# Kernel tuning notes

Measured on AMD Instinct MI355X. Metric: run time of the kernel, lower is better.

## Reference

```python
import jax, jax.numpy as jnp
import numpy as np

WS = 8        # window_size
NH = 16       # num_heads

def setup_inputs() -> dict:
    key = jax.random.key(0)
    ks = jax.random.split(key, 6)
    B, H, W, C = 16, 64, 64, 512
    nW = (H // WS) * (W // WS)
    return {
        "x": jax.random.normal(ks[0], (B, H * W, C), jnp.float32),
        "qkv_w": jax.random.normal(ks[1], (3 * C, C), jnp.float32) * 0.02,
        "qkv_b": jax.random.normal(ks[2], (3 * C,), jnp.float32) * 0.02,
        "proj_w": jax.random.normal(ks[3], (C, C), jnp.float32) * 0.02,
        "proj_b": jax.random.normal(ks[4], (C,), jnp.float32) * 0.02,
        "attn_mask": jax.random.normal(ks[5], (nW, WS * WS, WS * WS), jnp.float32),
        "H": H,
        "W": W,
    }

def reference(x, qkv_w, qkv_b, proj_w, proj_b, attn_mask, H, W):
    B, N, C = x.shape
    ws = WS
    hd = C // NH
    scale = hd ** (-0.5)
    x_img = x.reshape(B, H, W, C)
    pad_h = (ws - H % ws) % ws
    pad_w = (ws - W % ws) % ws
    if pad_h > 0 or pad_w > 0:
        x_img = jnp.pad(x_img, ((0, 0), (0, pad_h), (0, pad_w), (0, 0)))
    Hp, Wp = H + pad_h, W + pad_w
    nW = (Hp // ws) * (Wp // ws)
    # window partition: [B*nW, ws*ws, C]
    x_win = x_img.reshape(B, Hp // ws, ws, Wp // ws, ws, C)
    x_win = x_win.transpose(0, 1, 3, 2, 4, 5).reshape(B * nW, ws * ws, C)
    # fused qkv projection (torch Linear: y = x @ W^T + b)
    qkv = x_win @ qkv_w.T + qkv_b
    qkv = qkv.reshape(B * nW, ws * ws, 3, NH, hd).transpose(2, 0, 3, 1, 4)
    q, k, v = qkv[0], qkv[1], qkv[2]  # each [B*nW, NH, ws*ws, hd]
    attn = jnp.einsum('bhqd,bhkd->bhqk', q, k) * scale
    if attn_mask is not None:
        attn = attn.reshape(B, nW, NH, ws * ws, ws * ws)
        attn = attn + attn_mask[None, :, None, :, :]
        attn = attn.reshape(B * nW, NH, ws * ws, ws * ws)
    attn = jax.nn.softmax(attn, axis=-1)
    out = jnp.einsum('bhqk,bhkd->bhqd', attn, v)
    out = out.transpose(0, 2, 1, 3).reshape(B * nW, ws * ws, C)
    out = out @ proj_w.T + proj_b
    # window reverse
    out = out.reshape(B, Hp // ws, Wp // ws, ws, ws, C)
    out = out.transpose(0, 1, 3, 2, 4, 5).reshape(B, Hp, Wp, C)
    out = out[:, :H, :W, :].reshape(B, H * W, C)
    return out
```

## Files before the change

### kernel.cpp

```cpp
#include <hip/hip_runtime.h>


typedef unsigned short u16;
typedef unsigned int u32;
typedef __attribute__((ext_vector_type(8))) u16 u16x8;
typedef __attribute__((ext_vector_type(8))) short short8;
typedef __attribute__((ext_vector_type(4))) float f32x4;

__device__ __forceinline__ u16 f2bf(float f) {
    u32 u = __float_as_uint(f);
    u += 0x7fffu + ((u >> 16) & 1u);
    return (u16)(u >> 16);
}

__device__ __forceinline__ f32x4 MFMA(u16x8 a, u16x8 b, f32x4 c) {
    return __builtin_amdgcn_mfma_f32_16x16x32_bf16(
        __builtin_bit_cast(short8, a), __builtin_bit_cast(short8, b), c, 0, 0, 0);
}

__device__ __forceinline__ void gload16(const void* g, void* l) {
    __builtin_amdgcn_global_load_lds(
        (const __attribute__((address_space(1))) void*)g,
        (__attribute__((address_space(3))) void*)l, 16, 0, 0);
}

__device__ __forceinline__ int win2img(int r) {
    int b = r >> 12;
    int w = (r >> 6) & 63;
    int t = r & 63;
    int img = (((w >> 3) << 3) + (t >> 3)) * 64 + ((w & 7) << 3) + (t & 7);
    return (b << 12) + img;
}

__device__ __forceinline__ u16x8 cvt8(const float* src) {
    float4 a = *(const float4*)src;
    float4 b = *(const float4*)(src + 4);
    u16x8 t;
    t[0] = f2bf(a.x); t[1] = f2bf(a.y); t[2] = f2bf(a.z); t[3] = f2bf(a.w);
    t[4] = f2bf(b.x); t[5] = f2bf(b.y); t[6] = f2bf(b.z); t[7] = f2bf(b.w);
    return t;
}

__global__ __launch_bounds__(256)
void conv_f2b(const float* __restrict__ in, u16* __restrict__ out, int n8) {
    int u = blockIdx.x * 256 + threadIdx.x;
    if (u >= n8) return;
    *(u16x8*)(out + (size_t)u * 8) = cvt8(in + (size_t)u * 8);
}

__global__ __launch_bounds__(256)
void conv_permute_x(const float* __restrict__ x, u16* __restrict__ xw) {
    int u = blockIdx.x * 256 + threadIdx.x;
    int r = u >> 6;
    int c = (u & 63) << 3;
    int g = win2img(r);
    *(u16x8*)(xw + (size_t)r * 512 + c) = cvt8(x + (size_t)g * 512 + c);
}

template<bool PERM_OUT, bool OUT_F32>
__global__ __launch_bounds__(256, 4)
void gemm_bt(const u16* __restrict__ A, const u16* __restrict__ Wt,
             const float* __restrict__ bias, void* __restrict__ C,
             int NB, int Nfull)
{
    __shared__ char lds[32768];

    const int nwg = gridDim.x;
    const int q   = nwg >> 3;
    const int wg  = (blockIdx.x & 7) * q + (blockIdx.x >> 3);
    const int m0  = (wg / NB) * 128;
    const int n0  = (wg % NB) * 128;

    const int tid  = threadIdx.x;
    const int lane = tid & 63;
    const int wv   = tid >> 6;
    const int wm   = (wv >> 1) << 6;
    const int wn   = (wv & 1) << 6;
    const int lr   = lane & 15;
    const int lg   = lane >> 4;

    const int grow  = tid >> 2;
    const int gcolb = (tid & 3) << 4;
    const u32 tb    = (u32)tid << 4;

    const char* aptr = (const char*)A + (((size_t)(m0 + grow)) << 10) + gcolb;
    const char* bptr = (const char*)Wt + (((size_t)(n0 + grow)) << 10) + gcolb;

    f32x4 acc[4][4] = {};

#define STAGE(buf, kt) do {                                                   \
    const int ko_ = (kt) * 64;                                                \
    char* d_ = lds + (buf) * 16384 + tb;                                      \
    gload16(aptr + ko_,              d_);                                     \
    gload16(aptr + (64 << 10) + ko_, d_ + 4096);                              \
    gload16(bptr + ko_,              d_ + 8192);                              \
    gload16(bptr + (64 << 10) + ko_, d_ + 12288);                             \
} while (0)

#define COMPUTE(buf) do {                                                     \
    const u16* As_ = (const u16*)(lds + (buf) * 16384);                       \
    const u16* Bs_ = (const u16*)(lds + (buf) * 16384 + 8192);                \
    u16x8 af_[4], bf_[4];                                                     \
    _Pragma("unroll")                                                         \
    for (int mi = 0; mi < 4; ++mi)                                            \
        af_[mi] = *(const u16x8*)(As_ + (wm + mi * 16 + lr) * 32 + lg * 8);   \
    _Pragma("unroll")                                                         \
    for (int ni = 0; ni < 4; ++ni)                                            \
        bf_[ni] = *(const u16x8*)(Bs_ + (wn + ni * 16 + lr) * 32 + lg * 8);   \
    _Pragma("unroll")                                                         \
    for (int mi = 0; mi < 4; ++mi)                                            \
        _Pragma("unroll")                                                     \
        for (int ni = 0; ni < 4; ++ni)                                        \
            acc[mi][ni] = MFMA(af_[mi], bf_[ni], acc[mi][ni]);                \
} while (0)

    STAGE(0, 0);
    __syncthreads();

#pragma unroll 1
    for (int kt = 0; kt < 16; kt += 2) {
        STAGE(1, kt + 1);
        COMPUTE(0);
        __syncthreads();
        if (kt + 2 < 16) STAGE(0, kt + 2);
        COMPUTE(1);
        __syncthreads();
    }

#undef STAGE
#undef COMPUTE

#pragma unroll
    for (int mi = 0; mi < 4; ++mi) {
#pragma unroll
        for (int ni = 0; ni < 4; ++ni) {
            const int col = n0 + wn + ni * 16 + lr;
            const float bv = bias[col];
#pragma unroll
            for (int r = 0; r < 4; ++r) {
                int gr = m0 + wm + mi * 16 + lg * 4 + r;
                if (PERM_OUT) gr = win2img(gr);
                const float v = acc[mi][ni][r] + bv;
                if constexpr (OUT_F32)
                    ((float*)C)[(size_t)gr * Nfull + col] = v;
                else
                    ((u16*)C)[(size_t)gr * Nfull + col] = f2bf(v);
            }
        }
    }
}

__global__ __launch_bounds__(256, 2)
void attn_kernel(const u16* __restrict__ qkv, const float* __restrict__ mask,
                 u16* __restrict__ attn_out)
{
    __shared__ u16 sP[4][64][72];

    const int tid  = threadIdx.x;
    const int lane = tid & 63;
    const int wv   = tid >> 6;
    const int lr   = lane & 15;
    const int lg   = lane >> 4;
    const int win  = blockIdx.x;
    const int wib  = win & 63;
    const size_t rb = (size_t)win * 64;
    const float* maskp = mask + (size_t)wib * 64 * 64;
    const float scale = 0.17677669529663687f;

    for (int hi = 0; hi < 4; ++hi) {
        const int h = hi * 4 + wv;
        const size_t hoff = (size_t)h * 32;

        u16x8 qf[4], kf[4];
#pragma unroll
        for (int mt = 0; mt < 4; ++mt) {
            const u16* rowp = qkv + (rb + mt * 16 + lr) * 1536 + hoff + lg * 8;
            qf[mt] = *(const u16x8*)rowp;
            kf[mt] = *(const u16x8*)(rowp + 512);
        }
        f32x4 s[4][4] = {};
#pragma unroll
        for (int mi = 0; mi < 4; ++mi)
#pragma unroll
            for (int ni = 0; ni < 4; ++ni)
                s[mi][ni] = MFMA(qf[mi], kf[ni], s[mi][ni]);

        float rsum[4][4];
#pragma unroll
        for (int mi = 0; mi < 4; ++mi) {
#pragma unroll
            for (int r = 0; r < 4; ++r) {
                const int qrow = mi * 16 + lg * 4 + r;
                float vv[4];
                float mx = -1e30f;
#pragma unroll
                for (int ni = 0; ni < 4; ++ni) {
                    const int kcol = ni * 16 + lr;
                    float v = s[mi][ni][r] * scale + maskp[qrow * 64 + kcol];
                    vv[ni] = v;
                    mx = fmaxf(mx, v);
                }
#pragma unroll
                for (int mk = 1; mk <= 8; mk <<= 1)
                    mx = fmaxf(mx, __shfl_xor(mx, mk, 64));
                float sum = 0.f;
#pragma unroll
                for (int ni = 0; ni < 4; ++ni) {
                    float p = __expf(vv[ni] - mx);
                    sum += p;
                    s[mi][ni][r] = p;
                }
#pragma unroll
                for (int mk = 1; mk <= 8; mk <<= 1)
                    sum += __shfl_xor(sum, mk, 64);
                rsum[mi][r] = sum;
            }
        }

        __syncthreads();
#pragma unroll
        for (int mi = 0; mi < 4; ++mi)
#pragma unroll
            for (int ni = 0; ni < 4; ++ni)
#pragma unroll
                for (int r = 0; r < 4; ++r)
                    sP[wv][mi * 16 + lg * 4 + r][ni * 16 + lr] = f2bf(s[mi][ni][r]);
        __syncthreads();

        u16x8 pf[4][2];
#pragma unroll
        for (int mt = 0; mt < 4; ++mt)
#pragma unroll
            for (int k2 = 0; k2 < 2; ++k2)
                pf[mt][k2] = *(const u16x8*)&sP[wv][mt * 16 + lr][k2 * 32 + lg * 8];

        u16x8 vf[2][2];
#pragma unroll
        for (int k2 = 0; k2 < 2; ++k2)
#pragma unroll
            for (int nt = 0; nt < 2; ++nt) {
                const u16* vp = qkv + (rb + k2 * 32 + lg * 8) * 1536 + 1024 + hoff + nt * 16 + lr;
                u16x8 tmp;
#pragma unroll
                for (int j = 0; j < 8; ++j) tmp[j] = vp[(size_t)j * 1536];
                vf[k2][nt] = tmp;
            }

        f32x4 o[4][2] = {};
#pragma unroll
        for (int mt = 0; mt < 4; ++mt)
#pragma unroll
            for (int k2 = 0; k2 < 2; ++k2)
#pragma unroll
                for (int nt = 0; nt < 2; ++nt)
                    o[mt][nt] = MFMA(pf[mt][k2], vf[k2][nt], o[mt][nt]);

#pragma unroll
        for (int mt = 0; mt < 4; ++mt)
#pragma unroll
            for (int nt = 0; nt < 2; ++nt)
#pragma unroll
                for (int r = 0; r < 4; ++r) {
                    const int row = mt * 16 + lg * 4 + r;
                    const int d = nt * 16 + lr;
                    attn_out[(rb + row) * 512 + hoff + d] =
                        f2bf(o[mt][nt][r] / rsum[mt][r]);
                }
    }
}

extern "C" void kernel_launch(void* const* d_in, const int* in_sizes, int n_in,
                              void* d_out, int out_size, void* d_ws, size_t ws_size,
                              hipStream_t stream)
{
    const float* x      = (const float*)d_in[0];
    const float* qkv_w  = (const float*)d_in[1];
    const float* qkv_b  = (const float*)d_in[2];
    const float* proj_w = (const float*)d_in[3];
    const float* proj_b = (const float*)d_in[4];
    const float* mask   = (const float*)d_in[5];
    float* out = (float*)d_out;

    const size_t WQKV  = 1536ull * 512;
    const size_t WPROJ = 512ull * 512;

    u16* wq = (u16*)d_ws;
    u16* wp = wq + WQKV;
    u16* chunk = wp + WPROJ;

    const size_t xwPB  = 4096ull * 512;
    const size_t qkvPB = 4096ull * 1536;
    const size_t attPB = 4096ull * 512;
    const size_t perBatchBytes = (xwPB + qkvPB + attPB) * 2;

    size_t avail = ws_size - (WQKV + WPROJ) * 2;
    int Bc = (int)(avail / perBatchBytes);
    if (Bc > 16) Bc = 16;
    if (Bc < 1) Bc = 1;

    u16* xw_ws  = chunk;
    u16* qkv_ws = xw_ws + (size_t)Bc * xwPB;
    u16* att_ws = qkv_ws + (size_t)Bc * qkvPB;

    conv_f2b<<<dim3((WQKV / 8 + 255) / 256), 256, 0, stream>>>(qkv_w, wq, (int)(WQKV / 8));
    conv_f2b<<<dim3((WPROJ / 8 + 255) / 256), 256, 0, stream>>>(proj_w, wp, (int)(WPROJ / 8));

    for (int b0 = 0; b0 < 16; b0 += Bc) {
        const int bc = (16 - b0) < Bc ? (16 - b0) : Bc;
        const float* xc = x + (size_t)b0 * 4096 * 512;
        float* outc = out + (size_t)b0 * 4096 * 512;

        conv_permute_x<<<dim3(bc * 1024), 256, 0, stream>>>(xc, xw_ws);
        gemm_bt<false, false><<<dim3(bc * 32 * 12), 256, 0, stream>>>(
            xw_ws, wq, qkv_b, qkv_ws, 12, 1536);
        attn_kernel<<<dim3(bc * 64), 256, 0, stream>>>(qkv_ws, mask, att_ws);
        gemm_bt<true, true><<<dim3(bc * 32 * 4), 256, 0, stream>>>(
            att_ws, wp, proj_b, outc, 4, 512);
    }
}
```

Measured before the change: 332.0 us.

## Fuse x conversion into QKV GEMM, write V transposed, stage mask in LDS

Removes the separate conv_permute_x kernel. The QKV GEMM now loads fp32 x rows directly in window order, converts them to bf16 in registers and writes them to LDS, with a K tile of 32. The V part of the QKV output is written transposed per window, so the attention kernel can load V fragments with a single vector load instead of eight strided scalar loads. The attention kernel also stages the mask transposed in LDS and reads it as float4. The cost is that the fp32 A tile is re-read and re-converted by all 12 column blocks, which adds global traffic and an extra sync per K step.

```diff
diff --git a/kernel.cpp b/kernel.cpp
--- a/kernel.cpp
+++ b/kernel.cpp
@@ -3,6 +3,7 @@
 
 typedef unsigned short u16;
 typedef unsigned int u32;
+typedef __attribute__((ext_vector_type(4))) u16 u16x4;
 typedef __attribute__((ext_vector_type(8))) u16 u16x8;
 typedef __attribute__((ext_vector_type(8))) short short8;
 typedef __attribute__((ext_vector_type(4))) float f32x4;
@@ -48,28 +49,19 @@
     *(u16x8*)(out + (size_t)u * 8) = cvt8(in + (size_t)u * 8);
 }
 
-__global__ __launch_bounds__(256)
-void conv_permute_x(const float* __restrict__ x, u16* __restrict__ xw) {
-    int u = blockIdx.x * 256 + threadIdx.x;
-    int r = u >> 6;
-    int c = (u & 63) << 3;
-    int g = win2img(r);
-    *(u16x8*)(xw + (size_t)r * 512 + c) = cvt8(x + (size_t)g * 512 + c);
-}
-
-template<bool PERM_OUT, bool OUT_F32>
-__global__ __launch_bounds__(256, 4)
-void gemm_bt(const u16* __restrict__ A, const u16* __restrict__ Wt,
-             const float* __restrict__ bias, void* __restrict__ C,
-             int NB, int Nfull)
+__global__ __launch_bounds__(256, 3)
+void gemm_qkv(const float* __restrict__ X, const u16* __restrict__ Wq,
+              const float* __restrict__ bias, u16* __restrict__ QK,
+              u16* __restrict__ VT)
 {
-    __shared__ char lds[32768];
+    __shared__ u16 sA[2][128 * 32];
+    __shared__ u16 sB[2][128 * 32];
 
     const int nwg = gridDim.x;
     const int q   = nwg >> 3;
-    const int wg  = (blockIdx.x & 7) * q + (blockIdx.x >> 3);
-    const int m0  = (wg / NB) * 128;
-    const int n0  = (wg % NB) * 128;
+    const int wg  = ((int)blockIdx.x & 7) * q + ((int)blockIdx.x >> 3);
+    const int m0  = (wg / 12) * 128;
+    const int n0  = (wg % 12) * 128;
 
     const int tid  = threadIdx.x;
     const int lane = tid & 63;
@@ -79,12 +71,133 @@
     const int lr   = lane & 15;
     const int lg   = lane >> 4;
 
-    const int grow  = tid >> 2;
-    const int gcolb = (tid & 3) << 4;
-    const u32 tb    = (u32)tid << 4;
-
-    const char* aptr = (const char*)A + (((size_t)(m0 + grow)) << 10) + gcolb;
-    const char* bptr = (const char*)Wt + (((size_t)(n0 + grow)) << 10) + gcolb;
+    const int ar = tid >> 1;
+    const int kh = (tid & 1) << 4;
+    const float* ax = X + ((size_t)win2img(m0 + ar) << 9) + kh;
+    u16* aw = &sA[0][ar * 32 + kh];
+
+    const char* bptr0 = (const char*)Wq + ((size_t)(n0 + (tid >> 2)) << 10) + ((tid & 3) << 4);
+    const char* bptr1 = bptr0 + (64 << 10);
+
+    f32x4 acc[4][4] = {};
+    float4 a0, a1, a2, a3;
+
+#define LOADA(kt) do {                                                        \
+    const float* p_ = ax + (kt) * 32;                                         \
+    a0 = *(const float4*)p_;  a1 = *(const float4*)(p_ + 4);                  \
+    a2 = *(const float4*)(p_ + 8); a3 = *(const float4*)(p_ + 12);            \
+} while (0)
+
+#define WRITEA(buf) do {                                                      \
+    u16x8 t_;                                                                 \
+    t_[0]=f2bf(a0.x); t_[1]=f2bf(a0.y); t_[2]=f2bf(a0.z); t_[3]=f2bf(a0.w);   \
+    t_[4]=f2bf(a1.x); t_[5]=f2bf(a1.y); t_[6]=f2bf(a1.z); t_[7]=f2bf(a1.w);   \
+    *(u16x8*)(aw + (buf) * 4096) = t_;                                        \
+    t_[0]=f2bf(a2.x); t_[1]=f2bf(a2.y); t_[2]=f2bf(a2.z); t_[3]=f2bf(a2.w);   \
+    t_[4]=f2bf(a3.x); t_[5]=f2bf(a3.y); t_[6]=f2bf(a3.z); t_[7]=f2bf(a3.w);   \
+    *(u16x8*)(aw + (buf) * 4096 + 8) = t_;                                    \
+} while (0)
+
+#define STAGEB(buf, kt) do {                                                  \
+    char* d_ = (char*)sB + (buf) * 8192 + tid * 16;                           \
+    gload16(bptr0 + (kt) * 64, d_);                                           \
+    gload16(bptr1 + (kt) * 64, d_ + 4096);                                    \
+} while (0)
+
+#define COMPUTE(buf) do {                                                     \
+    const u16* As_ = &sA[buf][0];                                             \
+    const u16* Bs_ = &sB[buf][0];                                             \
+    u16x8 af_[4], bf_[4];                                                     \
+    _Pragma("unroll")                                                         \
+    for (int mi = 0; mi < 4; ++mi)                                            \
+        af_[mi] = *(const u16x8*)(As_ + (wm + mi * 16 + lr) * 32 + lg * 8);   \
+    _Pragma("unroll")                                                         \
+    for (int ni = 0; ni < 4; ++ni)                                            \
+        bf_[ni] = *(const u16x8*)(Bs_ + (wn + ni * 16 + lr) * 32 + lg * 8);   \
+    _Pragma("unroll")                                                         \
+    for (int mi = 0; mi < 4; ++mi)                                            \
+        _Pragma("unroll")                                                     \
+        for (int ni = 0; ni < 4; ++ni)                                        \
+            acc[mi][ni] = MFMA(af_[mi], bf_[ni], acc[mi][ni]);                \
+} while (0)
+
+    LOADA(0);
+    STAGEB(0, 0);
+    WRITEA(0);
+    __syncthreads();
+
+#pragma unroll 1
+    for (int t = 0; t < 16; ++t) {
+        const int cur = t & 1, nxt = cur ^ 1;
+        if (t < 15) { LOADA(t + 1); STAGEB(nxt, t + 1); }
+        COMPUTE(cur);
+        __syncthreads();
+        if (t < 15) {
+            WRITEA(nxt);
+            __syncthreads();
+        }
+    }
+
+#undef LOADA
+#undef WRITEA
+#undef STAGEB
+#undef COMPUTE
+
+    if (n0 < 1024) {
+#pragma unroll
+        for (int mi = 0; mi < 4; ++mi)
+#pragma unroll
+            for (int ni = 0; ni < 4; ++ni) {
+                const int col = n0 + wn + ni * 16 + lr;
+                const float bv = bias[col];
+#pragma unroll
+                for (int r = 0; r < 4; ++r) {
+                    const int gr = m0 + wm + mi * 16 + lg * 4 + r;
+                    QK[((size_t)gr << 10) + col] = f2bf(acc[mi][ni][r] + bv);
+                }
+            }
+    } else {
+#pragma unroll
+        for (int mi = 0; mi < 4; ++mi) {
+            const int gr0 = m0 + wm + mi * 16 + lg * 4;
+            const int win = gr0 >> 6, ro = gr0 & 63;
+#pragma unroll
+            for (int ni = 0; ni < 4; ++ni) {
+                const int col = n0 + wn + ni * 16 + lr;
+                const float bv = bias[col];
+                const int d = col - 1024;
+                u16x4 h;
+#pragma unroll
+                for (int r = 0; r < 4; ++r) h[r] = f2bf(acc[mi][ni][r] + bv);
+                *(u16x4*)(VT + (((size_t)win << 9) + d) * 64 + ro) = h;
+            }
+        }
+    }
+}
+
+__global__ __launch_bounds__(256, 4)
+void gemm_proj(const u16* __restrict__ A, const u16* __restrict__ Wt,
+               const float* __restrict__ bias, float* __restrict__ C)
+{
+    __shared__ char lds[32768];
+
+    const int nwg = gridDim.x;
+    const int q   = nwg >> 3;
+    const int wg  = ((int)blockIdx.x & 7) * q + ((int)blockIdx.x >> 3);
+    const int m0  = (wg / 4) * 128;
+    const int n0  = (wg % 4) * 128;
+
+    const int tid  = threadIdx.x;
+    const int lane = tid & 63;
+    const int wv   = tid >> 6;
+    const int wm   = (wv >> 1) << 6;
+    const int wn   = (wv & 1) << 6;
+    const int lr   = lane & 15;
+    const int lg   = lane >> 4;
+
+    const char* aptr = (const char*)A + (((size_t)(m0 + (tid >> 2))) << 10) + ((tid & 3) << 4);
+    const char* bptr = (const char*)Wt + (((size_t)(n0 + (tid >> 2))) << 10) + ((tid & 3) << 4);
+    const u32 tb = (u32)tid << 4;
 
     f32x4 acc[4][4] = {};
 
@@ -131,30 +244,25 @@
 #undef COMPUTE
 
 #pragma unroll
-    for (int mi = 0; mi < 4; ++mi) {
+    for (int mi = 0; mi < 4; ++mi)
 #pragma unroll
         for (int ni = 0; ni < 4; ++ni) {
             const int col = n0 + wn + ni * 16 + lr;
             const float bv = bias[col];
 #pragma unroll
             for (int r = 0; r < 4; ++r) {
-                int gr = m0 + wm + mi * 16 + lg * 4 + r;
-                if (PERM_OUT) gr = win2img(gr);
-                const float v = acc[mi][ni][r] + bv;
-                if constexpr (OUT_F32)
-                    ((float*)C)[(size_t)gr * Nfull + col] = v;
-                else
-                    ((u16*)C)[(size_t)gr * Nfull + col] = f2bf(v);
+                const int gr = win2img(m0 + wm + mi * 16 + lg * 4 + r);
+                C[((size_t)gr << 9) + col] = acc[mi][ni][r] + bv;
             }
         }
-    }
 }
 
 __global__ __launch_bounds__(256, 2)
-void attn_kernel(const u16* __restrict__ qkv, const float* __restrict__ mask,
-                 u16* __restrict__ attn_out)
+void attn_kernel(const u16* __restrict__ QK, const u16* __restrict__ VT,
+                 const float* __restrict__ mask, u16* __restrict__ attn_out)
 {
     __shared__ u16 sP[4][64][72];
+    __shared__ float mT[64 * 65];
 
     const int tid  = threadIdx.x;
     const int lane = tid & 63;
@@ -163,18 +271,31 @@
     const int lg   = lane >> 4;
     const int win  = blockIdx.x;
     const int wib  = win & 63;
-    const size_t rb = (size_t)win * 64;
-    const float* maskp = mask + (size_t)wib * 64 * 64;
+    const size_t rb = (size_t)win << 6;
     const float scale = 0.17677669529663687f;
+
+    {
+        const float* mp = mask + ((size_t)wib << 12) + tid * 16;
+        float4 v[4];
+#pragma unroll
+        for (int i = 0; i < 4; ++i) v[i] = *(const float4*)(mp + i * 4);
+        const int r0 = tid >> 2, c0 = (tid & 3) << 4;
+#pragma unroll
+        for (int e = 0; e < 16; ++e)
+            mT[(c0 + e) * 65 + r0] = v[e >> 2][e & 3];
+    }
+    __syncthreads();
+
+    const u16* vbase = VT + ((size_t)win << 15);
 
     for (int hi = 0; hi < 4; ++hi) {
         const int h = hi * 4 + wv;
-        const size_t hoff = (size_t)h * 32;
+        const int hoff = h * 32;
 
         u16x8 qf[4], kf[4];
 #pragma unroll
         for (int mt = 0; mt < 4; ++mt) {
-            const u16* rowp = qkv + (rb + mt * 16 + lr) * 1536 + hoff + lg * 8;
+            const u16* rowp = QK + ((rb + mt * 16 + lr) << 10) + hoff + lg * 8;
             qf[mt] = *(const u16x8*)rowp;
             kf[mt] = *(const u16x8*)(rowp + 512);
         }
@@ -188,15 +309,17 @@
         float rsum[4][4];
 #pragma unroll
         for (int mi = 0; mi < 4; ++mi) {
+            float4 mv[4];
+#pragma unroll
+            for (int ni = 0; ni < 4; ++ni)
+                mv[ni] = *(const float4*)&mT[(ni * 16 + lr) * 65 + mi * 16 + lg * 4];
 #pragma unroll
             for (int r = 0; r < 4; ++r) {
-                const int qrow = mi * 16 + lg * 4 + r;
                 float vv[4];
                 float mx = -1e30f;
 #pragma unroll
                 for (int ni = 0; ni < 4; ++ni) {
-                    const int kcol = ni * 16 + lr;
-                    float v = s[mi][ni][r] * scale + maskp[qrow * 64 + kcol];
+                    float v = s[mi][ni][r] * scale + ((const float*)&mv[ni])[r];
                     vv[ni] = v;
                     mx = fmaxf(mx, v);
                 }
@@ -238,13 +361,9 @@
 #pragma unroll
         for (int k2 = 0; k2 < 2; ++k2)
 #pragma unroll
-            for (int nt = 0; nt < 2; ++nt) {
-                const u16* vp = qkv + (rb + k2 * 32 + lg * 8) * 1536 + 1024 + hoff + nt * 16 + lr;
-                u16x8 tmp;
-#pragma unroll
-                for (int j = 0; j < 8; ++j) tmp[j] = vp[(size_t)j * 1536];
-                vf[k2][nt] = tmp;
-            }
+            for (int nt = 0; nt < 2; ++nt)
+                vf[k2][nt] = *(const u16x8*)(vbase
+                    + ((size_t)(hoff + nt * 16 + lr) << 6) + k2 * 32 + lg * 8);
 
         f32x4 o[4][2] = {};
 #pragma unroll
@@ -263,7 +382,7 @@
                 for (int r = 0; r < 4; ++r) {
                     const int row = mt * 16 + lg * 4 + r;
                     const int d = nt * 16 + lr;
-                    attn_out[(rb + row) * 512 + hoff + d] =
+                    attn_out[((rb + row) << 9) + hoff + d] =
                         f2bf(o[mt][nt][r] / rsum[mt][r]);
                 }
     }
@@ -288,19 +407,19 @@
     u16* wp = wq + WQKV;
     u16* chunk = wp + WPROJ;
 
-    const size_t xwPB  = 4096ull * 512;
-    const size_t qkvPB = 4096ull * 1536;
+    const size_t qkPB  = 4096ull * 1024;
+    const size_t vtPB  = 4096ull * 512;
     const size_t attPB = 4096ull * 512;
-    const size_t perBatchBytes = (xwPB + qkvPB + attPB) * 2;
+    const size_t perBatchBytes = (qkPB + vtPB + attPB) * 2;
 
     size_t avail = ws_size - (WQKV + WPROJ) * 2;
     int Bc = (int)(avail / perBatchBytes);
     if (Bc > 16) Bc = 16;
     if (Bc < 1) Bc = 1;
 
-    u16* xw_ws  = chunk;
-    u16* qkv_ws = xw_ws + (size_t)Bc * xwPB;
-    u16* att_ws = qkv_ws + (size_t)Bc * qkvPB;
+    u16* qk_ws  = chunk;
+    u16* vt_ws  = qk_ws + (size_t)Bc * qkPB;
+    u16* att_ws = vt_ws + (size_t)Bc * vtPB;
 
     conv_f2b<<<dim3((WQKV / 8 + 255) / 256), 256, 0, stream>>>(qkv_w, wq, (int)(WQKV / 8));
     conv_f2b<<<dim3((WPROJ / 8 + 255) / 256), 256, 0, stream>>>(proj_w, wp, (int)(WPROJ / 8));
@@ -310,11 +429,11 @@
         const float* xc = x + (size_t)b0 * 4096 * 512;
         float* outc = out + (size_t)b0 * 4096 * 512;
 
-        conv_permute_x<<<dim3(bc * 1024), 256, 0, stream>>>(xc, xw_ws);
-        gemm_bt<false, false><<<dim3(bc * 32 * 12), 256, 0, stream>>>(
-            xw_ws, wq, qkv_b, qkv_ws, 12, 1536);
-        attn_kernel<<<dim3(bc * 64), 256, 0, stream>>>(qkv_ws, mask, att_ws);
-        gemm_bt<true, true><<<dim3(bc * 32 * 4), 256, 0, stream>>>(
-            att_ws, wp, proj_b, outc, 4, 512);
-    }
-}
+        gemm_qkv<<<dim3(bc * 32 * 12), 256, 0, stream>>>(
+            xc, wq, qkv_b, qk_ws, vt_ws);
+        attn_kernel<<<dim3(bc * 64), 256, 0, stream>>>(
+            qk_ws, vt_ws, mask, att_ws);
+        gemm_proj<<<dim3(bc * 32 * 4), 256, 0, stream>>>(
+            att_ws, wp, proj_b, outc);
+    }
+}
```

Measured after the change: 370.3 us. +11.5%, slower.
